# Kernel tuning notes

Measured on AMD Instinct MI355X. Metric: run time of the kernel, lower is better.

Reference implementation:

```python
import jax, jax.numpy as jnp
import numpy as np

N_A, N_B = 30000, 30000
V, D_IN, D_OUT, H, E = 2, 128, 128, 4, 480000
EPS_LN = 1e-5


def setup_inputs() -> dict:
    key = jax.random.key(0)
    ks = jax.random.split(key, 22)
    rn = lambda i, sh, s=1.0: jax.random.normal(ks[i], sh, dtype=jnp.float32) * s
    ri = lambda i, n: jax.random.randint(ks[i], (E,), 0, n, dtype=jnp.int32)
    return {
        'feat_A': rn(0, (N_A, V, D_IN)),
        'feat_B': rn(1, (N_B, V, D_IN)),
        'src_ab': ri(2, N_A), 'dst_ab': ri(3, N_B),
        'val_ab': jax.random.uniform(ks[4], (E,), dtype=jnp.float32),
        'src_ba': ri(5, N_B), 'dst_ba': ri(6, N_A),
        'val_ba': jax.random.uniform(ks[7], (E,), dtype=jnp.float32),
        'W1': rn(8, (D_OUT, D_IN), 0.05), 'b1': jnp.zeros((D_OUT,), jnp.float32),
        'g1': jnp.ones((D_OUT,), jnp.float32), 'be1': jnp.zeros((D_OUT,), jnp.float32),
        'W2': rn(9, (D_OUT, D_IN), 0.05), 'b2': jnp.zeros((D_OUT,), jnp.float32),
        'g2': jnp.ones((D_OUT,), jnp.float32), 'be2': jnp.zeros((D_OUT,), jnp.float32),
        'Win': rn(10, (3 * D_OUT, D_OUT), 0.05), 'bin_': jnp.zeros((3 * D_OUT,), jnp.float32),
        'Wout': rn(11, (D_OUT, D_OUT), 0.05), 'bout': jnp.zeros((D_OUT,), jnp.float32),
        'lng': jnp.ones((D_OUT,), jnp.float32), 'lnb': jnp.zeros((D_OUT,), jnp.float32),
    }


def spmm_t(src, dst, val, h, n_out):
    # (adj^T @ h) over all views: h [N_src, V, d] -> [n_out, V, d]
    msg = h[src] * val[:, None, None]
    return jax.ops.segment_sum(msg, dst, num_segments=n_out)


def l2norm(x):
    n = jnp.sqrt(jnp.sum(x * x, axis=-1, keepdims=True))
    return x / jnp.maximum(n, 1e-12)


def layernorm(x, g, b):
    mu = jnp.mean(x, axis=-1, keepdims=True)
    var = jnp.mean((x - mu) ** 2, axis=-1, keepdims=True)
    return (x - mu) * jax.lax.rsqrt(var + EPS_LN) * g + b


def proj(x, W, b, g, be):
    # Linear -> LayerNorm -> ReLU
    return jax.nn.relu(layernorm(x @ W.T + b, g, be))


def mha(x, Win, bin_, Wout, bout, num_heads):
    # self-attention over the metapath axis P; x [..., P, d]
    *lead, P, d = x.shape
    dh = d // num_heads
    q, k, v = jnp.split(x @ Win.T + bin_, 3, axis=-1)
    hd = lambda t: t.reshape(*lead, P, num_heads, dh)
    q = hd(q) * (dh ** -0.5)
    scores = jnp.einsum('...qhe,...khe->...hqk', q, hd(k))
    a = jax.nn.softmax(scores, axis=-1)
    o = jnp.einsum('...hqk,...khe->...qhe', a, hd(v)).reshape(*lead, P, d)
    return o @ Wout.T + bout


def reference(feat_A, feat_B, src_ab, dst_ab, val_ab, src_ba, dst_ba, val_ba,
              W1, b1, g1, be1, W2, b2, g2, be2, Win, bin_, Wout, bout, lng, lnb):
    # metapath A->B->A
    h = l2norm(spmm_t(src_ab, dst_ab, val_ab, feat_A, N_B))
    h = l2norm(spmm_t(src_ba, dst_ba, val_ba, h, N_A))
    h1 = proj(h, W1, b1, g1, be1)                       # [N_A, V, d]
    # metapath B->A
    h = l2norm(spmm_t(src_ba, dst_ba, val_ba, feat_B, N_A))
    h2 = proj(h, W2, b2, g2, be2)                       # [N_A, V, d]
    x = jnp.stack([h1, h2], axis=2)                     # [N_A, V, P=2, d]
    attn = mha(x, Win, bin_, Wout, bout, H)
    y = layernorm(attn + x, lng, lnb).mean(axis=2)      # [N_A, V, d]
    return y  # h_global['A']; type B is identity passthrough of feat_B
```

## Files before the change

kernel.cpp:

```cpp
#include <hip/hip_runtime.h>

#define D 128
#define NODE_ROW 256

typedef __attribute__((ext_vector_type(8))) short short8;
typedef __attribute__((ext_vector_type(4))) float floatx4;

__device__ __forceinline__ ushort f2bf(float f) {
    unsigned int u = __float_as_uint(f);
    u += 0x7fffu + ((u >> 16) & 1u);
    return (ushort)(u >> 16);
}
__device__ __forceinline__ unsigned int pk2(float a, float b) {
    return (unsigned int)f2bf(a) | ((unsigned int)f2bf(b) << 16);
}
__device__ __forceinline__ float bf2f(ushort h) {
    return __uint_as_float(((unsigned int)h) << 16);
}
__device__ __forceinline__ short8 ldfrag(const ushort* p) {
    union { uint4 u; short8 s; } cv;
    cv.u = *(const uint4*)p;
    return cv.s;
}
__device__ __forceinline__ void acc4(float4& a, float w, uint2 u) {
    a.x += w * __uint_as_float(u.x << 16);
    a.y += w * __uint_as_float(u.x & 0xffff0000u);
    a.z += w * __uint_as_float(u.y << 16);
    a.w += w * __uint_as_float(u.y & 0xffff0000u);
}

__global__ __launch_bounds__(256) void k_f2b2(
    const float* __restrict__ srcA, const float* __restrict__ srcB,
    ushort* __restrict__ dstA, ushort* __restrict__ dstB, int n8) {
    int i = blockIdx.x * 256 + threadIdx.x;
    const float* s; ushort* d; int k;
    if (i < n8) { s = srcA; d = dstA; k = i; }
    else if (i < 2 * n8) { s = srcB; d = dstB; k = i - n8; }
    else return;
    const float4* sp = (const float4*)s + (size_t)k * 2;
    float4 a = sp[0], b = sp[1];
    uint4 o;
    o.x = pk2(a.x, a.y); o.y = pk2(a.z, a.w);
    o.z = pk2(b.x, b.y); o.w = pk2(b.z, b.w);
    ((uint4*)d)[k] = o;
}


__global__ __launch_bounds__(256) void k_hist(
    const int* __restrict__ dst_ab, const int* __restrict__ dst_ba,
    int* __restrict__ cnt_ab, int* __restrict__ cnt_ba, int E) {
    int i = blockIdx.x * 256 + threadIdx.x;
    if (i >= E) return;
    atomicAdd(&cnt_ab[dst_ab[i]], 1);
    atomicAdd(&cnt_ba[dst_ba[i]], 1);
}

__global__ __launch_bounds__(1024) void k_scan2(
    int* __restrict__ cntB, int* __restrict__ startB, int nB_,
    int* __restrict__ cntA, int* __restrict__ startA, int nA_) {
    __shared__ int part[1024];
    int* cnt; int* start; int n;
    if (blockIdx.x == 0) { cnt = cntB; start = startB; n = nB_; }
    else                 { cnt = cntA; start = startA; n = nA_; }
    int t = threadIdx.x;
    int chunk = (n + 1023) >> 10;
    int lo = min(t * chunk, n), hi = min(lo + chunk, n);
    int s = 0;
    for (int i = lo; i < hi; i++) s += cnt[i];
    part[t] = s;
    __syncthreads();
    for (int d = 1; d < 1024; d <<= 1) {
        int v = (t >= d) ? part[t - d] : 0;
        __syncthreads();
        part[t] += v;
        __syncthreads();
    }
    int off = part[t] - s;
    for (int i = lo; i < hi; i++) {
        int c = cnt[i];
        start[i] = off;
        cnt[i] = off;
        off += c;
    }
    if (t == 1023) start[n] = off;
}

__global__ __launch_bounds__(256) void k_scatter(
    const int* __restrict__ src_ab, const int* __restrict__ dst_ab,
    const float* __restrict__ val_ab,
    const int* __restrict__ src_ba, const int* __restrict__ dst_ba,
    const float* __restrict__ val_ba,
    int* __restrict__ cur_ab, int* __restrict__ cur_ba,
    int2* __restrict__ ep_ab, int2* __restrict__ ep_ba, int E) {
    int i = blockIdx.x * 256 + threadIdx.x;
    if (i >= E) return;
    {
        int pos = atomicAdd(&cur_ab[dst_ab[i]], 1);
        ep_ab[pos] = make_int2(src_ab[i], __float_as_int(val_ab[i]));
    }
    {
        int pos = atomicAdd(&cur_ba[dst_ba[i]], 1);
        ep_ba[pos] = make_int2(src_ba[i], __float_as_int(val_ba[i]));
    }
}

__global__ __launch_bounds__(256) void k_gather_norm_bf(
    const ushort* __restrict__ feat, const int2* __restrict__ ep,
    const int* __restrict__ start, ushort* __restrict__ out, int n) {
    int node = blockIdx.x * 4 + (threadIdx.x >> 6);
    if (node >= n) return;
    int lane = threadIdx.x & 63;
    int lo = start[node], hi = start[node + 1];
    float4 acc = make_float4(0.f, 0.f, 0.f, 0.f);
    int i = lo;
    for (; i + 3 < hi; i += 4) {
        int2 p0 = ep[i], p1 = ep[i + 1], p2 = ep[i + 2], p3 = ep[i + 3];
        uint2 u0 = ((const uint2*)(feat + (size_t)p0.x * NODE_ROW))[lane];
        uint2 u1 = ((const uint2*)(feat + (size_t)p1.x * NODE_ROW))[lane];
        uint2 u2 = ((const uint2*)(feat + (size_t)p2.x * NODE_ROW))[lane];
        uint2 u3 = ((const uint2*)(feat + (size_t)p3.x * NODE_ROW))[lane];
        acc4(acc, __int_as_float(p0.y), u0);
        acc4(acc, __int_as_float(p1.y), u1);
        acc4(acc, __int_as_float(p2.y), u2);
        acc4(acc, __int_as_float(p3.y), u3);
    }
    for (; i < hi; i++) {
        int2 p = ep[i];
        uint2 u = ((const uint2*)(feat + (size_t)p.x * NODE_ROW))[lane];
        acc4(acc, __int_as_float(p.y), u);
    }
    float ss = acc.x * acc.x + acc.y * acc.y + acc.z * acc.z + acc.w * acc.w;
    #pragma unroll
    for (int o = 16; o > 0; o >>= 1) ss += __shfl_xor(ss, o, 32);
    float sc = 1.0f / fmaxf(sqrtf(ss), 1e-12f);
    uint2 o;
    o.x = pk2(acc.x * sc, acc.y * sc);
    o.y = pk2(acc.z * sc, acc.w * sc);
    ((uint2*)(out + (size_t)node * NODE_ROW))[lane] = o;
}

__global__ __launch_bounds__(256) void k_cvt(
    const float* __restrict__ W1, const float* __restrict__ W2,
    const float* __restrict__ Win, const float* __restrict__ Wout,
    ushort* __restrict__ dst) {
    int idx = (blockIdx.x * 256 + threadIdx.x) * 4;
    if (idx >= 98304) return;
    const float* s; int off;
    if (idx < 16384)      { s = W1;  off = idx; }
    else if (idx < 32768) { s = W2;  off = idx - 16384; }
    else if (idx < 81920) { s = Win; off = idx - 32768; }
    else                  { s = Wout; off = idx - 81920; }
    float4 f = *(const float4*)(s + off);
    uint2 p;
    p.x = pk2(f.x, f.y);
    p.y = pk2(f.z, f.w);
    *(uint2*)(dst + idx) = p;
}

__global__ __launch_bounds__(256, 4) void k_tail(
    const ushort* __restrict__ hB, const ushort* __restrict__ fbB,
    const int2* __restrict__ ep, const int* __restrict__ start,
    const ushort* __restrict__ W1b, const float* __restrict__ b1,
    const float* __restrict__ g1, const float* __restrict__ be1,
    const ushort* __restrict__ W2b, const float* __restrict__ b2,
    const float* __restrict__ g2, const float* __restrict__ be2,
    const ushort* __restrict__ Winb, const float* __restrict__ binq,
    const ushort* __restrict__ Woutb, const float* __restrict__ bout,
    const float* __restrict__ lng, const float* __restrict__ lnb,
    float* __restrict__ out) {
    __shared__ __align__(16) char pool[34816];
    ushort (*xnP)[136] = (ushort(*)[136])(pool);
    ushort (*xnQ)[136] = (ushort(*)[136])(pool + 4352);
    ushort (*obuf)[140] = (ushort(*)[140])(pool);
    float (*ybP)[128] = (float(*)[128])(pool + 8960);
    float (*ybQ)[128] = (float(*)[128])(pool + 17152);
    float (*yy)[132]  = (float(*)[132])(pool + 8960);
    ushort (*xb)[136] = (ushort(*)[136])(pool + 25856);
    float* mu_s = (float*)(pool + 34560);
    float* rs_s = (float*)(pool + 34688);

    int t = threadIdx.x;
    int lane = t & 63, w = t >> 6;
    int c = lane & 15, quad = lane >> 4;
    int n0 = blockIdx.x * 8;
    size_t pairbase = (size_t)blockIdx.x * 16;

    #pragma unroll
    for (int nl = 0; nl < 2; nl++) {
        int node = n0 + w * 2 + nl;
        int lo = start[node], hi = start[node + 1];
        float4 aP = make_float4(0.f, 0.f, 0.f, 0.f);
        float4 aQ = make_float4(0.f, 0.f, 0.f, 0.f);
        int i = lo;
        for (; i + 3 < hi; i += 4) {
            int2 p0 = ep[i], p1 = ep[i + 1], p2 = ep[i + 2], p3 = ep[i + 3];
            size_t o0 = (size_t)p0.x * NODE_ROW, o1 = (size_t)p1.x * NODE_ROW;
            size_t o2 = (size_t)p2.x * NODE_ROW, o3 = (size_t)p3.x * NODE_ROW;
            uint2 uP0 = ((const uint2*)(hB + o0))[lane];
            uint2 uQ0 = ((const uint2*)(fbB + o0))[lane];
            uint2 uP1 = ((const uint2*)(hB + o1))[lane];
            uint2 uQ1 = ((const uint2*)(fbB + o1))[lane];
            uint2 uP2 = ((const uint2*)(hB + o2))[lane];
            uint2 uQ2 = ((const uint2*)(fbB + o2))[lane];
            uint2 uP3 = ((const uint2*)(hB + o3))[lane];
            uint2 uQ3 = ((const uint2*)(fbB + o3))[lane];
            float w0 = __int_as_float(p0.y), w1 = __int_as_float(p1.y);
            float w2 = __int_as_float(p2.y), w3 = __int_as_float(p3.y);
            acc4(aP, w0, uP0); acc4(aQ, w0, uQ0);
            acc4(aP, w1, uP1); acc4(aQ, w1, uQ1);
            acc4(aP, w2, uP2); acc4(aQ, w2, uQ2);
            acc4(aP, w3, uP3); acc4(aQ, w3, uQ3);
        }
        for (; i < hi; i++) {
            int2 p = ep[i];
            float wv = __int_as_float(p.y);
            size_t off = (size_t)p.x * NODE_ROW;
            uint2 uP = ((const uint2*)(hB + off))[lane];
            uint2 uQ = ((const uint2*)(fbB + off))[lane];
            acc4(aP, wv, uP); acc4(aQ, wv, uQ);
        }
        float ssP = aP.x * aP.x + aP.y * aP.y + aP.z * aP.z + aP.w * aP.w;
        float ssQ = aQ.x * aQ.x + aQ.y * aQ.y + aQ.z * aQ.z + aQ.w * aQ.w;
        #pragma unroll
        for (int o = 16; o > 0; o >>= 1) {
            ssP += __shfl_xor(ssP, o, 32);
            ssQ += __shfl_xor(ssQ, o, 32);
        }
        float scP = 1.0f / fmaxf(sqrtf(ssP), 1e-12f);
        float scQ = 1.0f / fmaxf(sqrtf(ssQ), 1e-12f);
        int rloc = (w * 2 + nl) * 2 + (lane >> 5);
        int col = (lane & 31) * 4;
        uint2 oP, oQ;
        oP.x = pk2(aP.x * scP, aP.y * scP); oP.y = pk2(aP.z * scP, aP.w * scP);
        oQ.x = pk2(aQ.x * scQ, aQ.y * scQ); oQ.y = pk2(aQ.z * scQ, aQ.w * scQ);
        *(uint2*)&xnP[rloc][col] = oP;
        *(uint2*)&xnQ[rloc][col] = oQ;
    }
    __syncthreads();

    {
        int set = w >> 1, wl = w & 1;
        const ushort* Wb = set ? W2b : W1b;
        const float* bb = set ? b2 : b1;
        ushort (*xn)[136] = set ? xnQ : xnP;
        float (*yb)[128] = set ? ybQ : ybP;
        short8 af[4];
        #pragma unroll
        for (int kt = 0; kt < 4; kt++)
            af[kt] = ldfrag(&xn[c][kt * 32 + quad * 8]);
        #pragma unroll
        for (int nt2 = 0; nt2 < 4; nt2++) {
            int j = (wl * 4 + nt2) * 16 + c;
            floatx4 acc = {0.f, 0.f, 0.f, 0.f};
            #pragma unroll
            for (int kt = 0; kt < 4; kt++) {
                short8 bfr = ldfrag(Wb + (size_t)j * 128 + kt * 32 + quad * 8);
                acc = __builtin_amdgcn_mfma_f32_16x16x32_bf16(af[kt], bfr, acc, 0, 0, 0);
            }
            float bj = bb[j];
            #pragma unroll
            for (int rg = 0; rg < 4; rg++)
                yb[quad * 4 + rg][j] = acc[rg] + bj;
        }
    }
    __syncthreads();

    {
        int set = t >> 7, tt = t & 127;
        int r = tt >> 3, ii = tt & 7;
        float (*yb)[128] = set ? ybQ : ybP;
        const float* gg = (set ? g2 : g1) + ii * 16;
        const float* bb = (set ? be2 : be1) + ii * 16;
        float v[16];
        const float* yr = &yb[r][ii * 16];
        #pragma unroll
        for (int e = 0; e < 16; e++) v[e] = yr[e];
        float s1 = 0.f, s2 = 0.f;
        #pragma unroll
        for (int e = 0; e < 16; e++) { s1 += v[e]; s2 += v[e] * v[e]; }
        s1 += __shfl_xor(s1, 1, 8); s2 += __shfl_xor(s2, 1, 8);
        s1 += __shfl_xor(s1, 2, 8); s2 += __shfl_xor(s2, 2, 8);
        s1 += __shfl_xor(s1, 4, 8); s2 += __shfl_xor(s2, 4, 8);
        float mu = s1 * (1.0f / 128.0f);
        float var = s2 * (1.0f / 128.0f) - mu * mu;
        float rs = rsqrtf(var + 1e-5f);
        float res[16];
        #pragma unroll
        for (int e = 0; e < 16; e++)
            res[e] = fmaxf((v[e] - mu) * rs * gg[e] + bb[e], 0.f);
        ushort* op = &xb[r * 2 + set][ii * 16];
        uint4 w0, w1;
        w0.x = pk2(res[0], res[1]);   w0.y = pk2(res[2], res[3]);
        w0.z = pk2(res[4], res[5]);   w0.w = pk2(res[6], res[7]);
        w1.x = pk2(res[8], res[9]);   w1.y = pk2(res[10], res[11]);
        w1.z = pk2(res[12], res[13]); w1.w = pk2(res[14], res[15]);
        ((uint4*)op)[0] = w0;
        ((uint4*)op)[1] = w1;
    }
    __syncthreads();

    int jb = w * 32 + c;
    {
        const float qs = 0.17677669529663687f;
        float bq0 = binq[jb];         float bq1 = binq[jb + 16];
        float bk0 = binq[jb + 128];   float bk1 = binq[jb + 144];
        float bv0 = binq[jb + 256];   float bv1 = binq[jb + 272];
        #pragma unroll
        for (int hf = 0; hf < 2; hf++) {
            int rb = hf * 16;
            short8 af[4];
            #pragma unroll
            for (int kt = 0; kt < 4; kt++)
                af[kt] = ldfrag(&xb[rb + c][kt * 32 + quad * 8]);
            floatx4 aq0 = {0.f,0.f,0.f,0.f}, aq1 = {0.f,0.f,0.f,0.f};
            floatx4 ak0 = {0.f,0.f,0.f,0.f}, ak1 = {0.f,0.f,0.f,0.f};
            floatx4 av0 = {0.f,0.f,0.f,0.f}, av1 = {0.f,0.f,0.f,0.f};
            #pragma unroll
            for (int kt = 0; kt < 4; kt++) {
                const ushort* wp = Winb + kt * 32 + quad * 8;
                short8 f0 = ldfrag(wp + (size_t)(jb)       * 128);
                short8 f1 = ldfrag(wp + (size_t)(jb + 16)  * 128);
                short8 f2 = ldfrag(wp + (size_t)(jb + 128) * 128);
                short8 f3 = ldfrag(wp + (size_t)(jb + 144) * 128);
                short8 f4 = ldfrag(wp + (size_t)(jb + 256) * 128);
                short8 f5 = ldfrag(wp + (size_t)(jb + 272) * 128);
                aq0 = __builtin_amdgcn_mfma_f32_16x16x32_bf16(af[kt], f0, aq0, 0, 0, 0);
                aq1 = __builtin_amdgcn_mfma_f32_16x16x32_bf16(af[kt], f1, aq1, 0, 0, 0);
                ak0 = __builtin_amdgcn_mfma_f32_16x16x32_bf16(af[kt], f2, ak0, 0, 0, 0);
                ak1 = __builtin_amdgcn_mfma_f32_16x16x32_bf16(af[kt], f3, ak1, 0, 0, 0);
                av0 = __builtin_amdgcn_mfma_f32_16x16x32_bf16(af[kt], f4, av0, 0, 0, 0);
                av1 = __builtin_amdgcn_mfma_f32_16x16x32_bf16(af[kt], f5, av1, 0, 0, 0);
            }
            #pragma unroll
            for (int rg = 0; rg < 4; rg++) {
                aq0[rg] = (aq0[rg] + bq0) * qs;
                aq1[rg] = (aq1[rg] + bq1) * qs;
                ak0[rg] += bk0;  ak1[rg] += bk1;
                av0[rg] += bv0;  av1[rg] += bv1;
            }
            #pragma unroll
            for (int pl = 0; pl < 2; pl++) {
                int r0 = 2 * pl, r1 = 2 * pl + 1;
                float p00 = aq0[r0] * ak0[r0] + aq1[r0] * ak1[r0];
                float p01 = aq0[r0] * ak0[r1] + aq1[r0] * ak1[r1];
                float p10 = aq0[r1] * ak0[r0] + aq1[r1] * ak1[r0];
                float p11 = aq0[r1] * ak0[r1] + aq1[r1] * ak1[r1];
                #pragma unroll
                for (int m = 1; m < 16; m <<= 1) {
                    p00 += __shfl_xor(p00, m, 16);
                    p01 += __shfl_xor(p01, m, 16);
                    p10 += __shfl_xor(p10, m, 16);
                    p11 += __shfl_xor(p11, m, 16);
                }
                float mx0 = fmaxf(p00, p01), mx1 = fmaxf(p10, p11);
                float e00 = __expf(p00 - mx0), e01 = __expf(p01 - mx0);
                float e10 = __expf(p10 - mx1), e11 = __expf(p11 - mx1);
                float i0 = 1.f / (e00 + e01), i1 = 1.f / (e10 + e11);
                float a00 = e00 * i0, a01 = e01 * i0;
                float a10 = e10 * i1, a11 = e11 * i1;
                float o00 = a00 * av0[r0] + a01 * av0[r1];
                float o10 = a10 * av0[r0] + a11 * av0[r1];
                float o01 = a00 * av1[r0] + a01 * av1[r1];
                float o11 = a10 * av1[r0] + a11 * av1[r1];
                int row0 = rb + quad * 4 + r0, row1 = rb + quad * 4 + r1;
                obuf[row0][jb]      = f2bf(o00);
                obuf[row1][jb]      = f2bf(o10);
                obuf[row0][jb + 16] = f2bf(o01);
                obuf[row1][jb + 16] = f2bf(o11);
            }
        }
    }
    __syncthreads();

    {
        #pragma unroll
        for (int hf = 0; hf < 2; hf++) {
            int rb = hf * 16;
            short8 af[4];
            #pragma unroll
            for (int kt = 0; kt < 4; kt++)
                af[kt] = ldfrag(&obuf[rb + c][kt * 32 + quad * 8]);
            #pragma unroll
            for (int nt2 = 0; nt2 < 2; nt2++) {
                int j = (w * 2 + nt2) * 16 + c;
                floatx4 acc = {0.f, 0.f, 0.f, 0.f};
                #pragma unroll
                for (int kt = 0; kt < 4; kt++) {
                    short8 bfr = ldfrag(Woutb + (size_t)j * 128 + kt * 32 + quad * 8);
                    acc = __builtin_amdgcn_mfma_f32_16x16x32_bf16(af[kt], bfr, acc, 0, 0, 0);
                }
                float bj = bout[j];
                #pragma unroll
                for (int rg = 0; rg < 4; rg++) {
                    int row = rb + quad * 4 + rg;
                    yy[row][j] = acc[rg] + bj + bf2f(xb[row][j]);
                }
            }
        }
    }
    __syncthreads();

    {
        int r = t >> 3, ii = t & 7;
        float s1 = 0.f, s2 = 0.f;
        const float* yr = &yy[r][ii * 16];
        #pragma unroll
        for (int cc = 0; cc < 16; cc++) { float v = yr[cc]; s1 += v; s2 += v * v; }
        s1 += __shfl_down(s1, 4, 8); s2 += __shfl_down(s2, 4, 8);
        s1 += __shfl_down(s1, 2, 8); s2 += __shfl_down(s2, 2, 8);
        s1 += __shfl_down(s1, 1, 8); s2 += __shfl_down(s2, 1, 8);
        if (ii == 0) {
            float mu = s1 / D;
            float var = s2 / D - mu * mu;
            mu_s[r] = mu; rs_s[r] = rsqrtf(var + 1e-5f);
        }
    }
    __syncthreads();

    if (t < 128) {
        int j = t;
        float gj = lng[j], bj = lnb[j];
        #pragma unroll
        for (int pp = 0; pp < 16; pp++) {
            int r0 = pp * 2, r1 = r0 + 1;
            float v0 = (yy[r0][j] - mu_s[r0]) * rs_s[r0] * gj + bj;
            float v1 = (yy[r1][j] - mu_s[r1]) * rs_s[r1] * gj + bj;
            out[(pairbase + pp) * D + j] = 0.5f * (v0 + v1);
        }
    }
}

extern "C" void kernel_launch(void* const* d_in, const int* in_sizes, int n_in,
                              void* d_out, int out_size, void* d_ws, size_t ws_size,
                              hipStream_t stream) {
    const float* feat_A = (const float*)d_in[0];
    const float* feat_B = (const float*)d_in[1];
    const int*   src_ab = (const int*)d_in[2];
    const int*   dst_ab = (const int*)d_in[3];
    const float* val_ab = (const float*)d_in[4];
    const int*   src_ba = (const int*)d_in[5];
    const int*   dst_ba = (const int*)d_in[6];
    const float* val_ba = (const float*)d_in[7];
    const float* W1 = (const float*)d_in[8];
    const float* b1 = (const float*)d_in[9];
    const float* g1 = (const float*)d_in[10];
    const float* be1 = (const float*)d_in[11];
    const float* W2 = (const float*)d_in[12];
    const float* b2 = (const float*)d_in[13];
    const float* g2 = (const float*)d_in[14];
    const float* be2 = (const float*)d_in[15];
    const float* Win = (const float*)d_in[16];
    const float* binq = (const float*)d_in[17];
    const float* Wout = (const float*)d_in[18];
    const float* bout = (const float*)d_in[19];
    const float* lng = (const float*)d_in[20];
    const float* lnb = (const float*)d_in[21];

    int E  = in_sizes[2];
    int nA = in_sizes[0] / NODE_ROW;
    int nB = in_sizes[1] / NODE_ROW;
    int rowsA = nA * 2;
    size_t nodeElems = (size_t)nA * NODE_ROW;

    ushort* fbA  = (ushort*)d_ws;
    ushort* fbB  = fbA + nodeElems;
    ushort* hB   = fbB + nodeElems;
    ushort* hA1  = hB + nodeElems;      (void)hA1;
    ushort* hA2  = hA1 + nodeElems;     (void)hA2;
    ushort* xbuf = hA2 + nodeElems;     (void)xbuf;
    ushort* Wbf  = xbuf + (size_t)rowsA * 2 * D;
    ushort* W1b   = Wbf;
    ushort* W2b   = Wbf + 16384;
    ushort* Winb  = Wbf + 32768;
    ushort* Woutb = Wbf + 81920;
    int* cnt_ab   = (int*)(Wbf + 98304);
    int* cnt_ba   = cnt_ab + nB;
    int* start_ab = cnt_ba + nA;
    int* start_ba = start_ab + (nB + 1);
    uintptr_t a = (uintptr_t)(start_ba + (nA + 1));
    a = (a + 15) & ~(uintptr_t)15;
    int2* ep_ab = (int2*)a;
    int2* ep_ba = ep_ab + E;

    int egrid = (E + 255) / 256;
    int n8 = (int)(nodeElems / 8);

    k_f2b2<<<(2 * n8 + 255) / 256, 256, 0, stream>>>(feat_A, feat_B, fbA, fbB, n8);

    hipMemsetAsync(cnt_ab, 0, (size_t)(nA + nB) * sizeof(int), stream);
    k_hist<<<egrid, 256, 0, stream>>>(dst_ab, dst_ba, cnt_ab, cnt_ba, E);
    k_scan2<<<2, 1024, 0, stream>>>(cnt_ab, start_ab, nB, cnt_ba, start_ba, nA);
    k_scatter<<<egrid, 256, 0, stream>>>(src_ab, dst_ab, val_ab,
                                         src_ba, dst_ba, val_ba,
                                         cnt_ab, cnt_ba, ep_ab, ep_ba, E);

    k_cvt<<<96, 256, 0, stream>>>(W1, W2, Win, Wout, Wbf);

    k_gather_norm_bf<<<(nB + 3) / 4, 256, 0, stream>>>(fbA, ep_ab, start_ab, hB, nB);

    k_tail<<<nA / 8, 256, 0, stream>>>(hB, fbB, ep_ba, start_ba,
                                       W1b, b1, g1, be1,
                                       W2b, b2, g2, be2,
                                       Winb, binq, Woutb, bout,
                                       lng, lnb, (float*)d_out);
}
```

Measured before the change: 546.3 us.

## Shrink k_tail shared memory by fusing projection LayerNorm into MFMA registers

The projection LayerNorm now works on MFMA accumulators held in registers. Row statistics are reduced with shuffles and a small shared array, so the fp32 ybP/ybQ staging buffers go away. The yy buffer is aliased onto the start of the pool, with an extra barrier before it is written. Together these cut the shared-memory pool from about 34 KB to about 18 KB, and launch bounds rise from 4 to 6 waves per SIMD to raise occupancy. The trade is higher register pressure, one more __syncthreads, and scattered 2-byte LDS stores for xb.

```diff
diff --git a/kernel.cpp b/kernel.cpp
--- a/kernel.cpp
+++ b/kernel.cpp
@@ -157,7 +157,7 @@
     *(uint2*)(dst + idx) = p;
 }
 
-__global__ __launch_bounds__(256, 4) void k_tail(
+__global__ __launch_bounds__(256, 6) void k_tail(
     const ushort* __restrict__ hB, const ushort* __restrict__ fbB,
     const int2* __restrict__ ep, const int* __restrict__ start,
     const ushort* __restrict__ W1b, const float* __restrict__ b1,
@@ -168,16 +168,15 @@
     const ushort* __restrict__ Woutb, const float* __restrict__ bout,
     const float* __restrict__ lng, const float* __restrict__ lnb,
     float* __restrict__ out) {
-    __shared__ __align__(16) char pool[34816];
+    __shared__ __align__(16) char pool[18432];
     ushort (*xnP)[136] = (ushort(*)[136])(pool);
     ushort (*xnQ)[136] = (ushort(*)[136])(pool + 4352);
     ushort (*obuf)[140] = (ushort(*)[140])(pool);
-    float (*ybP)[128] = (float(*)[128])(pool + 8960);
-    float (*ybQ)[128] = (float(*)[128])(pool + 17152);
-    float (*yy)[132]  = (float(*)[132])(pool + 8960);
-    ushort (*xb)[136] = (ushort(*)[136])(pool + 25856);
-    float* mu_s = (float*)(pool + 34560);
-    float* rs_s = (float*)(pool + 34688);
+    ushort (*xb)[136] = (ushort(*)[136])(pool + 8960);
+    float (*yy)[132]  = (float(*)[132])(pool);
+    float* stp  = (float*)(pool + 17664);
+    float* mu_s = (float*)(pool + 18176);
+    float* rs_s = (float*)(pool + 18304);
 
     int t = threadIdx.x;
     int lane = t & 63, w = t >> 6;
@@ -238,12 +237,12 @@
     }
     __syncthreads();
 
-    {
-        int set = w >> 1, wl = w & 1;
-        const ushort* Wb = set ? W2b : W1b;
-        const float* bb = set ? b2 : b1;
-        ushort (*xn)[136] = set ? xnQ : xnP;
-        float (*yb)[128] = set ? ybQ : ybP;
+    float yp[4][4];
+    int setp = w >> 1, wl = w & 1;
+    {
+        const ushort* Wb = setp ? W2b : W1b;
+        const float* bb = setp ? b2 : b1;
+        ushort (*xn)[136] = setp ? xnQ : xnP;
         short8 af[4];
         #pragma unroll
         for (int kt = 0; kt < 4; kt++)
@@ -260,42 +259,52 @@
             float bj = bb[j];
             #pragma unroll
             for (int rg = 0; rg < 4; rg++)
-                yb[quad * 4 + rg][j] = acc[rg] + bj;
-        }
-    }
-    __syncthreads();
-
-    {
-        int set = t >> 7, tt = t & 127;
-        int r = tt >> 3, ii = tt & 7;
-        float (*yb)[128] = set ? ybQ : ybP;
-        const float* gg = (set ? g2 : g1) + ii * 16;
-        const float* bb = (set ? be2 : be1) + ii * 16;
-        float v[16];
-        const float* yr = &yb[r][ii * 16];
-        #pragma unroll
-        for (int e = 0; e < 16; e++) v[e] = yr[e];
-        float s1 = 0.f, s2 = 0.f;
-        #pragma unroll
-        for (int e = 0; e < 16; e++) { s1 += v[e]; s2 += v[e] * v[e]; }
-        s1 += __shfl_xor(s1, 1, 8); s2 += __shfl_xor(s2, 1, 8);
-        s1 += __shfl_xor(s1, 2, 8); s2 += __shfl_xor(s2, 2, 8);
-        s1 += __shfl_xor(s1, 4, 8); s2 += __shfl_xor(s2, 4, 8);
-        float mu = s1 * (1.0f / 128.0f);
-        float var = s2 * (1.0f / 128.0f) - mu * mu;
-        float rs = rsqrtf(var + 1e-5f);
-        float res[16];
-        #pragma unroll
-        for (int e = 0; e < 16; e++)
-            res[e] = fmaxf((v[e] - mu) * rs * gg[e] + bb[e], 0.f);
-        ushort* op = &xb[r * 2 + set][ii * 16];
-        uint4 w0, w1;
-        w0.x = pk2(res[0], res[1]);   w0.y = pk2(res[2], res[3]);
-        w0.z = pk2(res[4], res[5]);   w0.w = pk2(res[6], res[7]);
-        w1.x = pk2(res[8], res[9]);   w1.y = pk2(res[10], res[11]);
-        w1.z = pk2(res[12], res[13]); w1.w = pk2(res[14], res[15]);
-        ((uint4*)op)[0] = w0;
-        ((uint4*)op)[1] = w1;
+                yp[nt2][rg] = acc[rg] + bj;
+        }
+        #pragma unroll
+        for (int rg = 0; rg < 4; rg++) {
+            float s1 = yp[0][rg] + yp[1][rg] + yp[2][rg] + yp[3][rg];
+            float s2 = yp[0][rg]*yp[0][rg] + yp[1][rg]*yp[1][rg]
+                     + yp[2][rg]*yp[2][rg] + yp[3][rg]*yp[3][rg];
+            s1 += __shfl_xor(s1, 1, 16); s2 += __shfl_xor(s2, 1, 16);
+            s1 += __shfl_xor(s1, 2, 16); s2 += __shfl_xor(s2, 2, 16);
+            s1 += __shfl_xor(s1, 4, 16); s2 += __shfl_xor(s2, 4, 16);
+            s1 += __shfl_xor(s1, 8, 16); s2 += __shfl_xor(s2, 8, 16);
+            if (c == 0) {
+                int row = quad * 4 + rg;
+                stp[((setp * 16 + row) * 2 + wl) * 2 + 0] = s1;
+                stp[((setp * 16 + row) * 2 + wl) * 2 + 1] = s2;
+            }
+        }
+    }
+    __syncthreads();
+
+    {
+        const float* gsrc = setp ? g2 : g1;
+        const float* bsrc = setp ? be2 : be1;
+        float ggv[4], bbv[4];
+        #pragma unroll
+        for (int nt2 = 0; nt2 < 4; nt2++) {
+            int j = (wl * 4 + nt2) * 16 + c;
+            ggv[nt2] = gsrc[j];
+            bbv[nt2] = bsrc[j];
+        }
+        #pragma unroll
+        for (int rg = 0; rg < 4; rg++) {
+            int row = quad * 4 + rg;
+            int base = ((setp * 16 + row) * 2) * 2;
+            float s1 = stp[base + 0] + stp[base + 2];
+            float s2 = stp[base + 1] + stp[base + 3];
+            float mu = s1 * (1.0f / 128.0f);
+            float var = s2 * (1.0f / 128.0f) - mu * mu;
+            float rs = rsqrtf(var + 1e-5f);
+            #pragma unroll
+            for (int nt2 = 0; nt2 < 4; nt2++) {
+                int j = (wl * 4 + nt2) * 16 + c;
+                float v = fmaxf((yp[nt2][rg] - mu) * rs * ggv[nt2] + bbv[nt2], 0.f);
+                xb[row * 2 + setp][j] = f2bf(v);
+            }
+        }
     }
     __syncthreads();
 
@@ -372,6 +381,7 @@
     }
     __syncthreads();
 
+    float y2[2][2][4];
     {
         #pragma unroll
         for (int hf = 0; hf < 2; hf++) {
@@ -393,8 +403,22 @@
                 #pragma unroll
                 for (int rg = 0; rg < 4; rg++) {
                     int row = rb + quad * 4 + rg;
-                    yy[row][j] = acc[rg] + bj + bf2f(xb[row][j]);
+                    y2[hf][nt2][rg] = acc[rg] + bj + bf2f(xb[row][j]);
                 }
+            }
+        }
+    }
+    __syncthreads();
+
+    {
+        #pragma unroll
+        for (int hf = 0; hf < 2; hf++) {
+            #pragma unroll
+            for (int nt2 = 0; nt2 < 2; nt2++) {
+                int j = (w * 2 + nt2) * 16 + c;
+                #pragma unroll
+                for (int rg = 0; rg < 4; rg++)
+                    yy[hf * 16 + quad * 4 + rg][j] = y2[hf][nt2][rg];
             }
         }
     }
```

New measurement: 524.9 us. 3.9% less time.
